# Kernel tuning notes

Hardware: AMD Instinct MI355X
Metric: run time of the kernel (lower is better)

The kernel has to match this reference:

```python
import jax, jax.numpy as jnp
import numpy as np

D = 768          # embedding_dim
H = 12           # num_heads
DH = 768         # head_dim == embedding_dim (hardcoded in Block)
DF = 4 * D       # FFN hidden
B, S = 4, 1024
EPS = 1e-5


def setup_inputs() -> dict:
    key = jax.random.key(0)
    ks = jax.random.split(key, 20)
    sd = lambda fan_in: 1.0 / np.sqrt(fan_in)
    return {
        "x":  jax.random.normal(ks[0], (B, S, D), jnp.float32),
        # per-head QKV (stacked over head axis)
        "Wq": jax.random.normal(ks[1], (H, D, DH), jnp.float32) * sd(D),
        "bq": jnp.zeros((H, DH), jnp.float32),
        "Wk": jax.random.normal(ks[2], (H, D, DH), jnp.float32) * sd(D),
        "bk": jnp.zeros((H, DH), jnp.float32),
        "Wv": jax.random.normal(ks[3], (H, D, DH), jnp.float32) * sd(D),
        "bv": jnp.zeros((H, DH), jnp.float32),
        # output projection: concat(H*DH) -> D
        "Wo": jax.random.normal(ks[4], (H * DH, D), jnp.float32) * sd(H * DH),
        "bo": jnp.zeros((D,), jnp.float32),
        # feed-forward
        "W1": jax.random.normal(ks[5], (D, DF), jnp.float32) * sd(D),
        "b1": jnp.zeros((DF,), jnp.float32),
        "W2": jax.random.normal(ks[6], (DF, D), jnp.float32) * sd(DF),
        "b2": jnp.zeros((D,), jnp.float32),
        # layer norms
        "g1": jnp.ones((D,), jnp.float32),  "be1": jnp.zeros((D,), jnp.float32),
        "g2": jnp.ones((D,), jnp.float32),  "be2": jnp.zeros((D,), jnp.float32),
    }


def _layernorm(x, g, b):
    mu = jnp.mean(x, axis=-1, keepdims=True)
    var = jnp.mean(jnp.square(x - mu), axis=-1, keepdims=True)
    return (x - mu) * jax.lax.rsqrt(var + EPS) * g + b


def reference(x, Wq, bq, Wk, bk, Wv, bv, Wo, bo, W1, b1, W2, b2, g1, be1, g2, be2):
    h = _layernorm(x, g1, be1)                                   # [B,S,D]
    # per-head projections, stacked over head axis -> [B,H,S,DH]
    Q = jnp.einsum('bsd,hde->bhse', h, Wq) + bq[None, :, None, :]
    K = jnp.einsum('bsd,hde->bhse', h, Wk) + bk[None, :, None, :]
    V = jnp.einsum('bsd,hde->bhse', h, Wv) + bv[None, :, None, :]
    scale = DH ** -0.5
    scores = jnp.einsum('bhse,bhte->bhst', Q, K) * scale          # [B,H,S,S] (no causal mask in source)
    attn = jax.nn.softmax(scores, axis=-1)
    ctx = jnp.einsum('bhst,bhte->bhse', attn, V)                  # [B,H,S,DH]
    concat = ctx.transpose(0, 2, 1, 3).reshape(B, S, H * DH)      # concat heads on last dim
    attn_out = concat @ Wo + bo                                   # dropout: eval identity
    x1 = x + attn_out
    h2 = _layernorm(x1, g2, be2)
    ffn = jax.nn.relu(h2 @ W1 + b1) @ W2 + b2                     # dropout: eval identity
    return x1 + ffn
```

## Files before the change

### kernel.cpp

```cpp
#include <hip/hip_runtime.h>
#include <hip/hip_bf16.h>


typedef __attribute__((ext_vector_type(8))) __bf16 bf16x8;
typedef __attribute__((ext_vector_type(4))) float f32x4;
typedef __attribute__((ext_vector_type(4))) float float4_t;
typedef __attribute__((ext_vector_type(4))) unsigned short ushort4_t;

#define DEV __device__ __forceinline__

DEV unsigned short f2bf(float f) {
    __hip_bfloat16 h = __float2bfloat16(f);
    return *reinterpret_cast<unsigned short*>(&h);
}
DEV float bf2f(unsigned short u) {
    return __uint_as_float(((unsigned int)u) << 16);
}

DEV void gld16(const void* g, void* l) {
    __builtin_amdgcn_global_load_lds(
        (const __attribute__((address_space(1))) void*)g,
        (__attribute__((address_space(3))) void*)l, 16, 0, 0);
}

__global__ __launch_bounds__(256) void f2b_conv(
    const float* __restrict__ in, unsigned short* __restrict__ outb, int n4)
{
    int i = blockIdx.x * 256 + threadIdx.x;
    if (i >= n4) return;
    float4_t v = *(const float4_t*)(in + (size_t)i * 4);
    ushort4_t o;
#pragma unroll
    for (int j = 0; j < 4; j++) o[j] = f2bf(v[j]);
    *(ushort4_t*)(outb + (size_t)i * 4) = o;
}

__global__ __launch_bounds__(256) void transpose_f2b(
    const float* __restrict__ in, unsigned short* __restrict__ outb, int R, int C)
{
    __shared__ float tile[32][33];
    const int c0 = blockIdx.x * 32, r0 = blockIdx.y * 32;
    const int tx = threadIdx.x & 31, ty = threadIdx.x >> 5;
#pragma unroll
    for (int i = 0; i < 32; i += 8)
        tile[ty + i][tx] = in[(size_t)(r0 + ty + i) * C + c0 + tx];
    __syncthreads();
#pragma unroll
    for (int i = 0; i < 32; i += 8)
        outb[(size_t)(c0 + ty + i) * R + r0 + tx] = f2bf(tile[tx][ty + i]);
}

__global__ __launch_bounds__(256) void wk_bq(
    const float* __restrict__ Wk, const float* __restrict__ bq, float* __restrict__ U)
{
    int i = blockIdx.x * 256 + threadIdx.x;
    int h = i / 768;
    const float* wr = Wk + (size_t)i * 768;
    const float* bh = bq + (size_t)h * 768;
    float s = 0.f;
#pragma unroll 4
    for (int e = 0; e < 768; e++) s += wr[e] * bh[e];
    U[i] = s;
}

__global__ __launch_bounds__(256) void bvwo_part(
    const float* __restrict__ Wo, const float* __restrict__ bv, float* __restrict__ part)
{
    int e = blockIdx.x * 256 + threadIdx.x;
    int r0 = blockIdx.y * 96;
    float s = 0.f;
#pragma unroll 4
    for (int r = r0; r < r0 + 96; r++) s += bv[r] * Wo[(size_t)r * 768 + e];
    part[(size_t)blockIdx.y * 768 + e] = s;
}

__global__ __launch_bounds__(256) void bvwo_final(
    const float* __restrict__ part, const float* __restrict__ bo, float* __restrict__ R)
{
    int e = blockIdx.x * 256 + threadIdx.x;
    float s = bo[e];
#pragma unroll
    for (int c = 0; c < 96; c++) s += part[(size_t)c * 768 + e];
    R[e] = s;
}

__global__ __launch_bounds__(256) void layernorm768(
    const float* __restrict__ in, const float* __restrict__ g,
    const float* __restrict__ be, unsigned short* __restrict__ outb)
{
    const size_t rowoff = (size_t)blockIdx.x * 768;
    const float* xr = in + rowoff;
    const int t = threadIdx.x;
    float v0 = xr[t], v1 = xr[t + 256], v2 = xr[t + 512];
    __shared__ float red[8];
    float s = v0 + v1 + v2;
#pragma unroll
    for (int o = 32; o; o >>= 1) s += __shfl_down(s, o);
    if ((t & 63) == 0) red[t >> 6] = s;
    __syncthreads();
    float mu = (red[0] + red[1] + red[2] + red[3]) * (1.0f / 768.0f);
    float d0 = v0 - mu, d1 = v1 - mu, d2 = v2 - mu;
    float q = d0 * d0 + d1 * d1 + d2 * d2;
#pragma unroll
    for (int o = 32; o; o >>= 1) q += __shfl_down(q, o);
    if ((t & 63) == 0) red[4 + (t >> 6)] = q;
    __syncthreads();
    float rs = rsqrtf((red[4] + red[5] + red[6] + red[7]) * (1.0f / 768.0f) + 1e-5f);
    outb[rowoff + t]       = f2bf(d0 * rs * g[t]       + be[t]);
    outb[rowoff + t + 256] = f2bf(d1 * rs * g[t + 256] + be[t + 256]);
    outb[rowoff + t + 512] = f2bf(d2 * rs * g[t + 512] + be[t + 512]);
}

__global__ __launch_bounds__(256) void softmax1024(unsigned short* __restrict__ p)
{
    unsigned short* row = p + (size_t)blockIdx.x * 1024;
    const int t = threadIdx.x;
    ushort4_t uv = *(const ushort4_t*)(row + t * 4);
    float v[4];
    float m = -3.4e38f;
#pragma unroll
    for (int i = 0; i < 4; i++) { v[i] = bf2f(uv[i]); m = fmaxf(m, v[i]); }
    __shared__ float red[8];
#pragma unroll
    for (int o = 32; o; o >>= 1) m = fmaxf(m, __shfl_down(m, o));
    if ((t & 63) == 0) red[t >> 6] = m;
    __syncthreads();
    m = fmaxf(fmaxf(red[0], red[1]), fmaxf(red[2], red[3]));
    float s = 0.f;
#pragma unroll
    for (int i = 0; i < 4; i++) { v[i] = __expf(v[i] - m); s += v[i]; }
#pragma unroll
    for (int o = 32; o; o >>= 1) s += __shfl_down(s, o);
    if ((t & 63) == 0) red[4 + (t >> 6)] = s;
    __syncthreads();
    float inv = 1.f / (red[4] + red[5] + red[6] + red[7]);
    ushort4_t ov;
#pragma unroll
    for (int i = 0; i < 4; i++) ov[i] = f2bf(v[i] * inv);
    *(ushort4_t*)(row + t * 4) = ov;
}

__global__ __launch_bounds__(256) void reduce2(
    const float* __restrict__ res, const float* __restrict__ colb,
    const float* __restrict__ p0, const float* __restrict__ p1,
    float* __restrict__ dst)
{
    int i = blockIdx.x * 256 + threadIdx.x;
    float4_t r = *(const float4_t*)(res + (size_t)i * 4);
    float4_t a = *(const float4_t*)(p0 + (size_t)i * 4);
    float4_t b = *(const float4_t*)(p1 + (size_t)i * 4);
    float4_t cb = *(const float4_t*)(colb + (size_t)(i % 192) * 4);
    float4_t o;
#pragma unroll
    for (int j = 0; j < 4; j++) o[j] = r[j] + cb[j] + a[j] + b[j];
    *(float4_t*)(dst + (size_t)i * 4) = o;
}

enum { MODE_BF16 = 0, MODE_VT = 1, MODE_F32RES = 2 };

template <int MODE, bool RELU>
__global__ __launch_bounds__(256) void gemm_bt(
    const unsigned short* __restrict__ A, int lda,
    const unsigned short* __restrict__ Bt, int ldb,
    void* __restrict__ Cout, int ldc,
    const float* __restrict__ bias,
    const float* __restrict__ res, int ldr,
    float scale, int K, int zdiv,
    long long sA1, long long sA2, long long sB1, long long sB2,
    long long sC1, long long sC2, long long sBias)
{
    const unsigned gx = gridDim.x, gy = gridDim.y;
    const unsigned nwg = gx * gy * gridDim.z;
    unsigned lin = blockIdx.x + gx * (blockIdx.y + gy * blockIdx.z);
    {
        const unsigned q = nwg >> 3, r = nwg & 7;
        const unsigned xcd = lin & 7, idx = lin >> 3;
        lin = (xcd < r ? xcd * (q + 1) : r * (q + 1) + (xcd - r) * q) + idx;
    }
    const unsigned bx = lin % gx;
    const unsigned rem = lin / gx;
    const unsigned by = rem % gy, bz = rem / gy;

    const int z = (int)bz, zq = z / zdiv, zr = z % zdiv;
    A  += (size_t)zq * sA1 + (size_t)zr * sA2;
    Bt += (size_t)zq * sB1 + (size_t)zr * sB2;
    const size_t cOff = (size_t)zq * sC1 + (size_t)zr * sC2;
    const float* biasp = bias ? bias + (size_t)zr * sBias : nullptr;

    const int m0 = by * 128, n0 = bx * 128;

    __shared__ __align__(16) unsigned short As[128 * 32];
    __shared__ __align__(16) unsigned short Bs[128 * 32];

    const int t = threadIdx.x, lane = t & 63, wave = t >> 6;
    const int wr = wave >> 1, wc = wave & 1;

    f32x4 zero = {0.f, 0.f, 0.f, 0.f};
    f32x4 acc[4][4];
#pragma unroll
    for (int i = 0; i < 4; i++)
#pragma unroll
        for (int j = 0; j < 4; j++) acc[i][j] = zero;

    const int r0 = t >> 2;
    const int ce = (t & 3) * 8;
    const int kq = (lane >> 4) * 8, rr = lane & 15;

    for (int k0 = 0; k0 < K; k0 += 32) {
        __syncthreads();
        {
            const unsigned short* ga0 = A  + (size_t)(m0 + r0) * lda      + k0 + ce;
            const unsigned short* ga1 = A  + (size_t)(m0 + 64 + r0) * lda + k0 + ce;
            const unsigned short* gb0 = Bt + (size_t)(n0 + r0) * ldb      + k0 + ce;
            const unsigned short* gb1 = Bt + (size_t)(n0 + 64 + r0) * ldb + k0 + ce;
            char* la = (char*)As;
            char* lb = (char*)Bs;
            gld16(ga0, la + wave * 1024);
            gld16(ga1, la + 4096 + wave * 1024);
            gld16(gb0, lb + wave * 1024);
            gld16(gb1, lb + 4096 + wave * 1024);
        }
        __syncthreads();

        bf16x8 a[4], b[4];
#pragma unroll
        for (int i = 0; i < 4; i++) {
            a[i] = *(const bf16x8*)(As + (wr * 64 + i * 16 + rr) * 32 + kq);
            b[i] = *(const bf16x8*)(Bs + (wc * 64 + i * 16 + rr) * 32 + kq);
        }
#pragma unroll
        for (int i = 0; i < 4; i++)
#pragma unroll
            for (int j = 0; j < 4; j++)
                acc[i][j] = __builtin_amdgcn_mfma_f32_16x16x32_bf16(a[i], b[j], acc[i][j], 0, 0, 0);
    }

    const int cr = (lane >> 4) * 4, cc = lane & 15;
#pragma unroll
    for (int i = 0; i < 4; i++) {
        const int rowb = m0 + wr * 64 + i * 16 + cr;
#pragma unroll
        for (int j = 0; j < 4; j++) {
            const int col = n0 + wc * 64 + j * 16 + cc;
            const float bv = biasp ? biasp[col] : 0.f;
            if (MODE == MODE_VT) {
                ushort4_t pk;
#pragma unroll
                for (int r = 0; r < 4; r++) {
                    float v = acc[i][j][r] * scale + bv;
                    if (RELU) v = fmaxf(v, 0.f);
                    pk[r] = f2bf(v);
                }
                *(ushort4_t*)((unsigned short*)Cout + cOff +
                              (size_t)col * ldc + rowb) = pk;
            } else {
#pragma unroll
                for (int r = 0; r < 4; r++) {
                    float v = acc[i][j][r] * scale + bv;
                    if (RELU) v = fmaxf(v, 0.f);
                    const int row = rowb + r;
                    if (MODE == MODE_BF16) {
                        ((unsigned short*)Cout)[cOff + (size_t)row * ldc + col] = f2bf(v);
                    } else {
                        float ov = res ? v + res[(size_t)row * ldr + col] : v;
                        ((float*)Cout)[cOff + (size_t)row * ldc + col] = ov;
                    }
                }
            }
        }
    }
}

__global__ void ws_too_small(float* o, float v) { o[0] = v; }

extern "C" void kernel_launch(void* const* d_in, const int* in_sizes, int n_in,
                              void* d_out, int out_size, void* d_ws, size_t ws_size,
                              hipStream_t stream)
{
    const float* x   = (const float*)d_in[0];
    const float* Wq  = (const float*)d_in[1];
    const float* bq  = (const float*)d_in[2];
    const float* Wk  = (const float*)d_in[3];
    const float* Wv  = (const float*)d_in[5];
    const float* bv  = (const float*)d_in[6];
    const float* Wo  = (const float*)d_in[7];
    const float* bo  = (const float*)d_in[8];
    const float* W1  = (const float*)d_in[9];
    const float* b1  = (const float*)d_in[10];
    const float* W2  = (const float*)d_in[11];
    const float* b2  = (const float*)d_in[12];
    const float* g1  = (const float*)d_in[13];
    const float* be1 = (const float*)d_in[14];
    const float* g2  = (const float*)d_in[15];
    const float* be2 = (const float*)d_in[16];
    float* out = (float*)d_out;

    char* ws = (char*)d_ws;
    unsigned short* W1T  = (unsigned short*)(ws);
    unsigned short* W2T  = (unsigned short*)(ws + 4718592);
    unsigned short* WQKT = (unsigned short*)(ws + 9437184);
    unsigned short* WVOT = (unsigned short*)(ws + 23592960);
    float*          U    = (float*)(ws + 37748736);
    float*          BVWO = (float*)(ws + 37785600);
    float*          PART = (float*)(ws + 37788672);
    unsigned short* HB   = (unsigned short*)(ws + 38083584);
    float*          X1   = (float*)(ws + 44375040);
    unsigned short* TB   = (unsigned short*)(ws + 56957952);
    unsigned short* SC   = (unsigned short*)(ws + 132455424);
    const size_t NEED = 233118720;

    if (ws_size < NEED) {
        hipMemsetAsync(d_out, 0, (size_t)out_size * sizeof(float), stream);
        ws_too_small<<<1, 1, 0, stream>>>(out, (float)ws_size);
        return;
    }

    unsigned short* VOT = TB;
    float* P0 = (float*)(ws + 9437184);
    float* P1 = (float*)(ws + 22020096);
    unsigned short* WqB = (unsigned short*)(ws + 132455424);
    unsigned short* WkB = (unsigned short*)(ws + 146611200);
    unsigned short* WvB = (unsigned short*)(ws + 160766976);
    unsigned short* WOT = (unsigned short*)(ws + 174922752);
    unsigned short* H2B = (unsigned short*)(ws + 56957952);
    unsigned short* FFN = (unsigned short*)(ws + 63249408);

    f2b_conv<<<6912, 256, 0, stream>>>(Wq, WqB, 1769472);
    f2b_conv<<<6912, 256, 0, stream>>>(Wk, WkB, 1769472);
    f2b_conv<<<6912, 256, 0, stream>>>(Wv, WvB, 1769472);
    transpose_f2b<<<dim3(24, 288), 256, 0, stream>>>(Wo, WOT, 9216, 768);
    transpose_f2b<<<dim3(96, 24), 256, 0, stream>>>(W1, W1T, 768, 3072);
    transpose_f2b<<<dim3(24, 96), 256, 0, stream>>>(W2, W2T, 3072, 768);

    gemm_bt<MODE_BF16, false><<<dim3(6, 6, 12), 256, 0, stream>>>(
        WkB, 768, WqB, 768, WQKT, 768, nullptr, nullptr, 0, 1.0f, 768, 12,
        0, 589824, 0, 589824, 0, 589824, 0);
    gemm_bt<MODE_BF16, false><<<dim3(6, 6, 12), 256, 0, stream>>>(
        WOT, 9216, WvB, 768, WVOT, 768, nullptr, nullptr, 0, 1.0f, 768, 12,
        0, 768, 0, 589824, 0, 589824, 0);

    wk_bq<<<36, 256, 0, stream>>>(Wk, bq, U);
    bvwo_part<<<dim3(3, 96), 256, 0, stream>>>(Wo, bv, PART);
    bvwo_final<<<3, 256, 0, stream>>>(PART, bo, BVWO);

    layernorm768<<<4096, 256, 0, stream>>>(x, g1, be1, HB);

    gemm_bt<MODE_BF16, false><<<dim3(6, 8, 48), 256, 0, stream>>>(
        HB, 768, WQKT, 768, TB, 768, U, nullptr, 0, 1.0f, 768, 12,
        786432, 0, 0, 589824, 9437184, 786432, 768);

    gemm_bt<MODE_BF16, false><<<dim3(8, 8, 48), 256, 0, stream>>>(
        TB, 768, HB, 768, SC, 12288, nullptr, nullptr, 0,
        0.03608439182435161f, 768, 12,
        9437184, 786432, 786432, 0, 12582912, 1024, 0);

    softmax1024<<<49152, 256, 0, stream>>>(SC);

    gemm_bt<MODE_VT, false><<<dim3(6, 8, 48), 256, 0, stream>>>(
        HB, 768, WVOT, 768, VOT, 12288, nullptr, nullptr, 0, 1.0f, 768, 12,
        786432, 0, 0, 589824, 9437184, 1024, 0);

    gemm_bt<MODE_F32RES, false><<<dim3(6, 8, 8), 256, 0, stream>>>(
        SC, 12288, VOT, 12288, P0, 768, nullptr, nullptr, 0, 1.0f, 6144, 4,
        6144, 12582912, 6144, 9437184, 3145728, 786432, 0);

    reduce2<<<3072, 256, 0, stream>>>(x, BVWO, P0, P1, X1);

    layernorm768<<<4096, 256, 0, stream>>>(X1, g2, be2, H2B);

    gemm_bt<MODE_BF16, true><<<dim3(24, 32, 1), 256, 0, stream>>>(
        H2B, 768, W1T, 768, FFN, 3072, b1, nullptr, 0, 1.0f, 768, 1,
        0, 0, 0, 0, 0, 0, 0);

    gemm_bt<MODE_F32RES, false><<<dim3(6, 32, 2), 256, 0, stream>>>(
        FFN, 3072, W2T, 3072, P0, 768, nullptr, nullptr, 0, 1.0f, 1536, 1,
        1536, 0, 1536, 0, 3145728, 0, 0);

    reduce2<<<3072, 256, 0, stream>>>(X1, b2, P0, P1, out);
}
```

Baseline: 758.3 us.

## Double-buffer GEMM LDS tiles and split-K four ways for PV and FFN2

Result: faster. 673.6 us (-11.2%).

```diff
diff --git a/kernel.cpp b/kernel.cpp
--- a/kernel.cpp
+++ b/kernel.cpp
@@ -140,19 +140,22 @@
     *(ushort4_t*)(row + t * 4) = ov;
 }
 
-__global__ __launch_bounds__(256) void reduce2(
+__global__ __launch_bounds__(256) void reduce4(
     const float* __restrict__ res, const float* __restrict__ colb,
     const float* __restrict__ p0, const float* __restrict__ p1,
+    const float* __restrict__ p2, const float* __restrict__ p3,
     float* __restrict__ dst)
 {
     int i = blockIdx.x * 256 + threadIdx.x;
     float4_t r = *(const float4_t*)(res + (size_t)i * 4);
     float4_t a = *(const float4_t*)(p0 + (size_t)i * 4);
     float4_t b = *(const float4_t*)(p1 + (size_t)i * 4);
+    float4_t c = *(const float4_t*)(p2 + (size_t)i * 4);
+    float4_t d = *(const float4_t*)(p3 + (size_t)i * 4);
     float4_t cb = *(const float4_t*)(colb + (size_t)(i % 192) * 4);
     float4_t o;
 #pragma unroll
-    for (int j = 0; j < 4; j++) o[j] = r[j] + cb[j] + a[j] + b[j];
+    for (int j = 0; j < 4; j++) o[j] = r[j] + cb[j] + (a[j] + b[j]) + (c[j] + d[j]);
     *(float4_t*)(dst + (size_t)i * 4) = o;
 }
 
@@ -167,7 +170,7 @@
     const float* __restrict__ res, int ldr,
     float scale, int K, int zdiv,
     long long sA1, long long sA2, long long sB1, long long sB2,
-    long long sC1, long long sC2, long long sBias)
+    long long sC1, long long sC2, long long sCJ, long long sBias)
 {
     const unsigned gx = gridDim.x, gy = gridDim.y;
     const unsigned nwg = gx * gy * gridDim.z;
@@ -184,13 +187,13 @@
     const int z = (int)bz, zq = z / zdiv, zr = z % zdiv;
     A  += (size_t)zq * sA1 + (size_t)zr * sA2;
     Bt += (size_t)zq * sB1 + (size_t)zr * sB2;
-    const size_t cOff = (size_t)zq * sC1 + (size_t)zr * sC2;
+    const size_t cOff = (size_t)zq * sC1 + (size_t)(zq >> 1) * sCJ + (size_t)zr * sC2;
     const float* biasp = bias ? bias + (size_t)zr * sBias : nullptr;
 
     const int m0 = by * 128, n0 = bx * 128;
 
-    __shared__ __align__(16) unsigned short As[128 * 32];
-    __shared__ __align__(16) unsigned short Bs[128 * 32];
+    __shared__ __align__(16) unsigned short As[2][128 * 32];
+    __shared__ __align__(16) unsigned short Bs[2][128 * 32];
 
     const int t = threadIdx.x, lane = t & 63, wave = t >> 6;
     const int wr = wave >> 1, wc = wave & 1;
@@ -206,33 +209,53 @@
     const int ce = (t & 3) * 8;
     const int kq = (lane >> 4) * 8, rr = lane & 15;
 
-    for (int k0 = 0; k0 < K; k0 += 32) {
-        __syncthreads();
-        {
-            const unsigned short* ga0 = A  + (size_t)(m0 + r0) * lda      + k0 + ce;
-            const unsigned short* ga1 = A  + (size_t)(m0 + 64 + r0) * lda + k0 + ce;
-            const unsigned short* gb0 = Bt + (size_t)(n0 + r0) * ldb      + k0 + ce;
-            const unsigned short* gb1 = Bt + (size_t)(n0 + 64 + r0) * ldb + k0 + ce;
-            char* la = (char*)As;
-            char* lb = (char*)Bs;
-            gld16(ga0, la + wave * 1024);
-            gld16(ga1, la + 4096 + wave * 1024);
-            gld16(gb0, lb + wave * 1024);
-            gld16(gb1, lb + 4096 + wave * 1024);
+    const int nt = K >> 5;
+
+    auto stage = [&](int buf, int kt) {
+        const int kk = kt * 32;
+        const unsigned short* ga0 = A  + (size_t)(m0 + r0) * lda      + kk + ce;
+        const unsigned short* ga1 = A  + (size_t)(m0 + 64 + r0) * lda + kk + ce;
+        const unsigned short* gb0 = Bt + (size_t)(n0 + r0) * ldb      + kk + ce;
+        const unsigned short* gb1 = Bt + (size_t)(n0 + 64 + r0) * ldb + kk + ce;
+        char* la = (char*)(&As[buf][0]);
+        char* lb = (char*)(&Bs[buf][0]);
+        gld16(ga0, la + wave * 1024);
+        gld16(ga1, la + 4096 + wave * 1024);
+        gld16(gb0, lb + wave * 1024);
+        gld16(gb1, lb + 4096 + wave * 1024);
+    };
+
+    stage(0, 0);
+    stage(1, 1);
+    asm volatile("s_waitcnt vmcnt(4)" ::: "memory");
+    __builtin_amdgcn_s_barrier();
+
+    int cur = 0;
+    for (int kt = 0; kt < nt; ++kt) {
+        bf16x8 a[4], b[4];
+        const unsigned short* Ab = &As[cur][0];
+        const unsigned short* Bb = &Bs[cur][0];
+#pragma unroll
+        for (int i = 0; i < 4; i++) {
+            a[i] = *(const bf16x8*)(Ab + (wr * 64 + i * 16 + rr) * 32 + kq);
+            b[i] = *(const bf16x8*)(Bb + (wc * 64 + i * 16 + rr) * 32 + kq);
         }
-        __syncthreads();
-
-        bf16x8 a[4], b[4];
-#pragma unroll
-        for (int i = 0; i < 4; i++) {
-            a[i] = *(const bf16x8*)(As + (wr * 64 + i * 16 + rr) * 32 + kq);
-            b[i] = *(const bf16x8*)(Bs + (wc * 64 + i * 16 + rr) * 32 + kq);
-        }
+        asm volatile("s_waitcnt lgkmcnt(0)" ::: "memory");
+        __builtin_amdgcn_s_barrier();
+        if (kt + 2 < nt) stage(cur, kt + 2);
+
+        __builtin_amdgcn_s_setprio(1);
 #pragma unroll
         for (int i = 0; i < 4; i++)
 #pragma unroll
             for (int j = 0; j < 4; j++)
                 acc[i][j] = __builtin_amdgcn_mfma_f32_16x16x32_bf16(a[i], b[j], acc[i][j], 0, 0, 0);
+        __builtin_amdgcn_s_setprio(0);
+
+        if (kt + 2 < nt) asm volatile("s_waitcnt vmcnt(4)" ::: "memory");
+        else             asm volatile("s_waitcnt vmcnt(0)" ::: "memory");
+        __builtin_amdgcn_s_barrier();
+        cur ^= 1;
     }
 
     const int cr = (lane >> 4) * 4, cc = lane & 15;
@@ -307,7 +330,7 @@
     float*          X1   = (float*)(ws + 44375040);
     unsigned short* TB   = (unsigned short*)(ws + 56957952);
     unsigned short* SC   = (unsigned short*)(ws + 132455424);
-    const size_t NEED = 233118720;
+    const size_t NEED = 258284544;
 
     if (ws_size < NEED) {
         hipMemsetAsync(d_out, 0, (size_t)out_size * sizeof(float), stream);
@@ -318,6 +341,8 @@
     unsigned short* VOT = TB;
     float* P0 = (float*)(ws + 9437184);
     float* P1 = (float*)(ws + 22020096);
+    float* P2 = (float*)(ws + 233118720);
+    float* P3 = (float*)(ws + 245701632);
     unsigned short* WqB = (unsigned short*)(ws + 132455424);
     unsigned short* WkB = (unsigned short*)(ws + 146611200);
     unsigned short* WvB = (unsigned short*)(ws + 160766976);
@@ -334,10 +359,10 @@
 
     gemm_bt<MODE_BF16, false><<<dim3(6, 6, 12), 256, 0, stream>>>(
         WkB, 768, WqB, 768, WQKT, 768, nullptr, nullptr, 0, 1.0f, 768, 12,
-        0, 589824, 0, 589824, 0, 589824, 0);
+        0, 589824, 0, 589824, 0, 589824, 0, 0);
     gemm_bt<MODE_BF16, false><<<dim3(6, 6, 12), 256, 0, stream>>>(
         WOT, 9216, WvB, 768, WVOT, 768, nullptr, nullptr, 0, 1.0f, 768, 12,
-        0, 768, 0, 589824, 0, 589824, 0);
+        0, 768, 0, 589824, 0, 589824, 0, 0);
 
     wk_bq<<<36, 256, 0, stream>>>(Wk, bq, U);
     bvwo_part<<<dim3(3, 96), 256, 0, stream>>>(Wo, bv, PART);
@@ -347,34 +372,34 @@
 
     gemm_bt<MODE_BF16, false><<<dim3(6, 8, 48), 256, 0, stream>>>(
         HB, 768, WQKT, 768, TB, 768, U, nullptr, 0, 1.0f, 768, 12,
-        786432, 0, 0, 589824, 9437184, 786432, 768);
+        786432, 0, 0, 589824, 9437184, 786432, 0, 768);
 
     gemm_bt<MODE_BF16, false><<<dim3(8, 8, 48), 256, 0, stream>>>(
         TB, 768, HB, 768, SC, 12288, nullptr, nullptr, 0,
         0.03608439182435161f, 768, 12,
-        9437184, 786432, 786432, 0, 12582912, 1024, 0);
+        9437184, 786432, 786432, 0, 12582912, 1024, 0, 0);
 
     softmax1024<<<49152, 256, 0, stream>>>(SC);
 
     gemm_bt<MODE_VT, false><<<dim3(6, 8, 48), 256, 0, stream>>>(
         HB, 768, WVOT, 768, VOT, 12288, nullptr, nullptr, 0, 1.0f, 768, 12,
-        786432, 0, 0, 589824, 9437184, 1024, 0);
-
-    gemm_bt<MODE_F32RES, false><<<dim3(6, 8, 8), 256, 0, stream>>>(
-        SC, 12288, VOT, 12288, P0, 768, nullptr, nullptr, 0, 1.0f, 6144, 4,
-        6144, 12582912, 6144, 9437184, 3145728, 786432, 0);
-
-    reduce2<<<3072, 256, 0, stream>>>(x, BVWO, P0, P1, X1);
+        786432, 0, 0, 589824, 9437184, 1024, 0, 0);
+
+    gemm_bt<MODE_F32RES, false><<<dim3(6, 8, 16), 256, 0, stream>>>(
+        SC, 12288, VOT, 12288, P0, 768, nullptr, nullptr, 0, 1.0f, 3072, 4,
+        3072, 12582912, 3072, 9437184, 3145728, 786432, 49628928, 0);
+
+    reduce4<<<3072, 256, 0, stream>>>(x, BVWO, P0, P1, P2, P3, X1);
 
     layernorm768<<<4096, 256, 0, stream>>>(X1, g2, be2, H2B);
 
     gemm_bt<MODE_BF16, true><<<dim3(24, 32, 1), 256, 0, stream>>>(
         H2B, 768, W1T, 768, FFN, 3072, b1, nullptr, 0, 1.0f, 768, 1,
-        0, 0, 0, 0, 0, 0, 0);
-
-    gemm_bt<MODE_F32RES, false><<<dim3(6, 32, 2), 256, 0, stream>>>(
-        FFN, 3072, W2T, 3072, P0, 768, nullptr, nullptr, 0, 1.0f, 1536, 1,
-        1536, 0, 1536, 0, 3145728, 0, 0);
-
-    reduce2<<<3072, 256, 0, stream>>>(X1, b2, P0, P1, out);
-}
+        0, 0, 0, 0, 0, 0, 0, 0);
+
+    gemm_bt<MODE_F32RES, false><<<dim3(6, 32, 4), 256, 0, stream>>>(
+        FFN, 3072, W2T, 3072, P0, 768, nullptr, nullptr, 0, 1.0f, 768, 1,
+        768, 0, 768, 0, 3145728, 0, 49628928, 0);
+
+    reduce4<<<3072, 256, 0, stream>>>(X1, b2, P0, P1, P2, P3, out);
+}
```
